# Kernel tuning notes

Measured on AMD Instinct MI355X. Metric: run time of the kernel, lower is better.

The kernel has to match this reference:

```python
import jax, jax.numpy as jnp
import numpy as np

BN_EPS = 1e-5


def _spe_forward(feature, neigh_idx, W, gamma, beta, running_mean, running_var):
    # feature: [B, C, N, 1]; neigh_idx: [B, N, K]
    B = feature.shape[0]
    pc = jnp.transpose(feature[..., 0], (0, 2, 1))            # [B, N, C]
    # gather neighbor features: [B, N, K, C]
    f_neigh = pc[jnp.arange(B)[:, None, None], neigh_idx]
    f_neigh = jnp.transpose(f_neigh, (0, 3, 1, 2))            # [B, C, N, K]
    f = jnp.concatenate((feature, f_neigh), axis=-1)          # [B, C, N, K+1]
    # 1x1 conv (no bias, followed by BN)
    h = jnp.einsum('oc,bcnk->bonk', W, f)                     # [B, O, N, K+1]
    # BatchNorm2d (eval mode with running stats) + ReLU
    inv = gamma / jnp.sqrt(running_var + BN_EPS)
    h = h * inv[None, :, None, None] + (beta - running_mean * inv)[None, :, None, None]
    h = jax.nn.relu(h)
    # sum over the neighbor axis, keepdim
    return jnp.sum(h, axis=-1, keepdims=True)                 # [B, O, N, 1]


def setup_inputs() -> dict:
    key = jax.random.key(0)
    k1, k2, k3 = jax.random.split(key, 3)
    B, C, N, K, O = 2, 64, 32768, 16, 64
    feature = jax.random.normal(k1, (B, C, N, 1), dtype=jnp.float32)
    neigh_idx = jax.random.randint(k2, (B, N, K), 0, N, dtype=jnp.int32)
    W = jax.random.normal(k3, (O, C), dtype=jnp.float32) * (1.0 / np.sqrt(C))
    gamma = jnp.ones((O,), dtype=jnp.float32)
    beta = jnp.zeros((O,), dtype=jnp.float32)
    running_mean = jnp.zeros((O,), dtype=jnp.float32)
    running_var = jnp.ones((O,), dtype=jnp.float32)
    return {"feature": feature, "neigh_idx": neigh_idx, "W": W,
            "gamma": gamma, "beta": beta,
            "running_mean": running_mean, "running_var": running_var}


def reference(feature, neigh_idx, W, gamma, beta, running_mean, running_var):
    return _spe_forward(feature, neigh_idx, W, gamma, beta, running_mean, running_var)
```

## Files before the change

kernel.cpp:

```cpp
#include <hip/hip_runtime.h>

#define BN_EPS 1e-5f

constexpr int Bb = 2;
constexpr int Cc = 64;
constexpr int Nn = 32768;
constexpr int Kk = 16;
constexpr int Oo = 64;

typedef __attribute__((ext_vector_type(8))) short v8s;
typedef __attribute__((ext_vector_type(4))) float v4f;

__device__ __forceinline__ unsigned short f2bf(float f) {
    unsigned u = __float_as_uint(f);
    return (unsigned short)((u + 0x7FFFu + ((u >> 16) & 1u)) >> 16);
}
__device__ __forceinline__ float bf2f(unsigned short h) {
    return __uint_as_float(((unsigned)h) << 16);
}

__global__ __launch_bounds__(256) void spe_gemm_mfma(
    const float* __restrict__ feature, const float* __restrict__ W,
    const float* __restrict__ gamma, const float* __restrict__ beta,
    const float* __restrict__ rmean, const float* __restrict__ rvar,
    unsigned short* __restrict__ t)
{
    __shared__ unsigned short fA[64][68];
    __shared__ unsigned short fB[64][68];
    const int tid = threadIdx.x;
    const int blk = blockIdx.x;
    const int b   = blk & 1;
    const int n0  = (blk >> 1) << 6;

    {
        const int nl = tid & 63;
        const int h  = tid >> 6;
        const float* fp = feature + (size_t)b * Cc * Nn + n0 + nl;
        #pragma unroll
        for (int i = 0; i < 16; ++i) {
            const int c = h * 16 + i;
            fA[nl][c] = f2bf(fp[(size_t)c * Nn]);
        }
        const int c2 = tid & 63;
        #pragma unroll
        for (int i = 0; i < 16; ++i) {
            const int o = h + i * 4;
            fB[o][c2] = f2bf(W[o * 64 + c2]);
        }
    }
    __syncthreads();

    const int wv   = tid >> 6;
    const int lane = tid & 63;
    const int q    = lane >> 4;
    const int r16  = lane & 15;

    union U8 { ushort4 u4[2]; v8s v; };
    const int am = wv * 16 + r16;
    U8 a0, a1;
    a0.u4[0] = *(const ushort4*)&fA[am][q * 8];
    a0.u4[1] = *(const ushort4*)&fA[am][q * 8 + 4];
    a1.u4[0] = *(const ushort4*)&fA[am][32 + q * 8];
    a1.u4[1] = *(const ushort4*)&fA[am][32 + q * 8 + 4];

    v4f acc[4];
    #pragma unroll
    for (int ot = 0; ot < 4; ++ot) {
        const int bo = ot * 16 + r16;
        U8 b0, b1;
        b0.u4[0] = *(const ushort4*)&fB[bo][q * 8];
        b0.u4[1] = *(const ushort4*)&fB[bo][q * 8 + 4];
        b1.u4[0] = *(const ushort4*)&fB[bo][32 + q * 8];
        b1.u4[1] = *(const ushort4*)&fB[bo][32 + q * 8 + 4];
        v4f c = {0.f, 0.f, 0.f, 0.f};
        c = __builtin_amdgcn_mfma_f32_16x16x32_bf16(a0.v, b0.v, c, 0, 0, 0);
        c = __builtin_amdgcn_mfma_f32_16x16x32_bf16(a1.v, b1.v, c, 0, 0, 0);
        acc[ot] = c;
    }

    #pragma unroll
    for (int ot = 0; ot < 4; ++ot) {
        const int o = ot * 16 + r16;
        const float inv  = gamma[o] / sqrtf(rvar[o] + BN_EPS);
        const float bias = beta[o] - rmean[o] * inv;
        unsigned short* tp = t + ((size_t)b * Nn + n0 + wv * 16 + q * 4) * 64 + o;
        #pragma unroll
        for (int r = 0; r < 4; ++r)
            tp[(size_t)r * 64] = f2bf(fmaxf(fmaf(inv, acc[ot][r], bias), 0.0f));
    }
}

__global__ __launch_bounds__(1024) void spe_gather_sum(
    const unsigned short* __restrict__ t, const int* __restrict__ idx,
    float* __restrict__ out)
{
    __shared__ float s[64 * 65];
    const int tid  = threadIdx.x;
    const int wv   = tid >> 6;
    const int lane = tid & 63;
    const int p    = lane >> 4;
    const int q    = lane & 15;
    const int blk  = blockIdx.x;
    const int b    = blk & 1;
    const int n0   = ((blk >> 1) & 511) << 6;
    const int ng   = n0 + wv * 4;

    const unsigned short* tb = t + (size_t)b * Nn * 64;

    const int myidx = idx[((size_t)b * Nn + ng) * Kk + lane];

    const int n = ng + p;
    const ushort4 c4 = *(const ushort4*)&tb[(size_t)n * 64 + q * 4];
    float ax = bf2f(c4.x), ay = bf2f(c4.y), az = bf2f(c4.z), aw = bf2f(c4.w);
    #pragma unroll
    for (int j = 0; j < 16; ++j) {
        const int nj = __shfl(myidx, p * 16 + j);
        const ushort4 v = *(const ushort4*)&tb[(size_t)nj * 64 + q * 4];
        ax += bf2f(v.x); ay += bf2f(v.y); az += bf2f(v.z); aw += bf2f(v.w);
    }

    const int nl = wv * 4 + p;
    float* sp = &s[nl * 65 + q * 4];
    sp[0] = ax; sp[1] = ay; sp[2] = az; sp[3] = aw;
    __syncthreads();

    const int nl2 = tid & 63;
    const int ob  = tid >> 6;
    float* op = out + (size_t)b * Oo * Nn + n0 + nl2;
    #pragma unroll
    for (int i = 0; i < 4; ++i) {
        const int o = ob * 4 + i;
        op[(size_t)o * Nn] = s[nl2 * 65 + o];
    }
}

extern "C" void kernel_launch(void* const* d_in, const int* in_sizes, int n_in,
                              void* d_out, int out_size, void* d_ws, size_t ws_size,
                              hipStream_t stream) {
    const float* feature = (const float*)d_in[0];
    const int*   nidx    = (const int*)d_in[1];
    const float* W       = (const float*)d_in[2];
    const float* gamma   = (const float*)d_in[3];
    const float* beta    = (const float*)d_in[4];
    const float* rmean   = (const float*)d_in[5];
    const float* rvar    = (const float*)d_in[6];
    float* out = (float*)d_out;
    unsigned short* t = (unsigned short*)d_ws;

    const int nblocks = Bb * (Nn / 64);
    spe_gemm_mfma<<<nblocks, 256, 0, stream>>>(feature, W, gamma, beta, rmean, rvar, t);
    spe_gather_sum<<<nblocks, 1024, 0, stream>>>(t, nidx, out);
}
```

Baseline: 95.53 us.

## Load GEMM operands directly to registers and widen gather rows to 16 bytes

The GEMM kernel no longer stages feature and W through shared memory. Each lane loads its MFMA fragments straight from global memory, with swapped operand roles so that output rows are written as packed ushort4 stores, and the BN parameters are read as float4. The gather kernel now uses 512 threads with 8 lanes per point, each lane loading 16-byte rows, and issues all 17 loads before accumulating to raise memory-level parallelism. This trades shared-memory staging and a barrier for more redundant global reads of W and higher register pressure from holding 17 uint4 values per lane.

```diff
diff --git a/kernel.cpp b/kernel.cpp
--- a/kernel.cpp
+++ b/kernel.cpp
@@ -15,9 +15,6 @@
     unsigned u = __float_as_uint(f);
     return (unsigned short)((u + 0x7FFFu + ((u >> 16) & 1u)) >> 16);
 }
-__device__ __forceinline__ float bf2f(unsigned short h) {
-    return __uint_as_float(((unsigned)h) << 16);
-}
 
 __global__ __launch_bounds__(256) void spe_gemm_mfma(
     const float* __restrict__ feature, const float* __restrict__ W,
@@ -25,72 +22,62 @@
     const float* __restrict__ rmean, const float* __restrict__ rvar,
     unsigned short* __restrict__ t)
 {
-    __shared__ unsigned short fA[64][68];
-    __shared__ unsigned short fB[64][68];
     const int tid = threadIdx.x;
     const int blk = blockIdx.x;
     const int b   = blk & 1;
     const int n0  = (blk >> 1) << 6;
-
-    {
-        const int nl = tid & 63;
-        const int h  = tid >> 6;
-        const float* fp = feature + (size_t)b * Cc * Nn + n0 + nl;
-        #pragma unroll
-        for (int i = 0; i < 16; ++i) {
-            const int c = h * 16 + i;
-            fA[nl][c] = f2bf(fp[(size_t)c * Nn]);
-        }
-        const int c2 = tid & 63;
-        #pragma unroll
-        for (int i = 0; i < 16; ++i) {
-            const int o = h + i * 4;
-            fB[o][c2] = f2bf(W[o * 64 + c2]);
-        }
-    }
-    __syncthreads();
 
     const int wv   = tid >> 6;
     const int lane = tid & 63;
     const int q    = lane >> 4;
     const int r16  = lane & 15;
 
-    union U8 { ushort4 u4[2]; v8s v; };
-    const int am = wv * 16 + r16;
-    U8 a0, a1;
-    a0.u4[0] = *(const ushort4*)&fA[am][q * 8];
-    a0.u4[1] = *(const ushort4*)&fA[am][q * 8 + 4];
-    a1.u4[0] = *(const ushort4*)&fA[am][32 + q * 8];
-    a1.u4[1] = *(const ushort4*)&fA[am][32 + q * 8 + 4];
+    union U { ushort4 u4[2]; unsigned short us[8]; v8s v; };
 
-    v4f acc[4];
+    const int nb = n0 + wv * 16 + r16;
+    const float* fp = feature + (size_t)b * Cc * Nn + nb;
+    U bf0, bf1;
     #pragma unroll
-    for (int ot = 0; ot < 4; ++ot) {
-        const int bo = ot * 16 + r16;
-        U8 b0, b1;
-        b0.u4[0] = *(const ushort4*)&fB[bo][q * 8];
-        b0.u4[1] = *(const ushort4*)&fB[bo][q * 8 + 4];
-        b1.u4[0] = *(const ushort4*)&fB[bo][32 + q * 8];
-        b1.u4[1] = *(const ushort4*)&fB[bo][32 + q * 8 + 4];
-        v4f c = {0.f, 0.f, 0.f, 0.f};
-        c = __builtin_amdgcn_mfma_f32_16x16x32_bf16(a0.v, b0.v, c, 0, 0, 0);
-        c = __builtin_amdgcn_mfma_f32_16x16x32_bf16(a1.v, b1.v, c, 0, 0, 0);
-        acc[ot] = c;
+    for (int jj = 0; jj < 8; ++jj) {
+        bf0.us[jj] = f2bf(fp[(size_t)(q * 8 + jj) * Nn]);
+        bf1.us[jj] = f2bf(fp[(size_t)(q * 8 + jj + 32) * Nn]);
     }
 
     #pragma unroll
     for (int ot = 0; ot < 4; ++ot) {
-        const int o = ot * 16 + r16;
-        const float inv  = gamma[o] / sqrtf(rvar[o] + BN_EPS);
-        const float bias = beta[o] - rmean[o] * inv;
-        unsigned short* tp = t + ((size_t)b * Nn + n0 + wv * 16 + q * 4) * 64 + o;
+        const int oa = ot * 16 + r16;
+        const float* wp = W + oa * 64 + q * 8;
+        U af0, af1;
         #pragma unroll
-        for (int r = 0; r < 4; ++r)
-            tp[(size_t)r * 64] = f2bf(fmaxf(fmaf(inv, acc[ot][r], bias), 0.0f));
+        for (int jj = 0; jj < 8; ++jj) {
+            af0.us[jj] = f2bf(wp[jj]);
+            af1.us[jj] = f2bf(wp[jj + 32]);
+        }
+        v4f c = {0.f, 0.f, 0.f, 0.f};
+        c = __builtin_amdgcn_mfma_f32_16x16x32_bf16(af0.v, bf0.v, c, 0, 0, 0);
+        c = __builtin_amdgcn_mfma_f32_16x16x32_bf16(af1.v, bf1.v, c, 0, 0, 0);
+
+        const int ob4 = ot * 16 + q * 4;
+        const float4 g4  = *(const float4*)&gamma[ob4];
+        const float4 be4 = *(const float4*)&beta[ob4];
+        const float4 m4  = *(const float4*)&rmean[ob4];
+        const float4 v4  = *(const float4*)&rvar[ob4];
+        float inv[4], bias[4];
+        inv[0] = g4.x / sqrtf(v4.x + BN_EPS);  bias[0] = be4.x - m4.x * inv[0];
+        inv[1] = g4.y / sqrtf(v4.y + BN_EPS);  bias[1] = be4.y - m4.y * inv[1];
+        inv[2] = g4.z / sqrtf(v4.z + BN_EPS);  bias[2] = be4.z - m4.z * inv[2];
+        inv[3] = g4.w / sqrtf(v4.w + BN_EPS);  bias[3] = be4.w - m4.w * inv[3];
+
+        ushort4 ov;
+        ov.x = f2bf(fmaxf(fmaf(inv[0], c[0], bias[0]), 0.0f));
+        ov.y = f2bf(fmaxf(fmaf(inv[1], c[1], bias[1]), 0.0f));
+        ov.z = f2bf(fmaxf(fmaf(inv[2], c[2], bias[2]), 0.0f));
+        ov.w = f2bf(fmaxf(fmaf(inv[3], c[3], bias[3]), 0.0f));
+        *(ushort4*)&t[((size_t)b * Nn + nb) * 64 + ob4] = ov;
     }
 }
 
-__global__ __launch_bounds__(1024) void spe_gather_sum(
+__global__ __launch_bounds__(512, 4) void spe_gather_sum(
     const unsigned short* __restrict__ t, const int* __restrict__ idx,
     float* __restrict__ out)
 {
@@ -98,38 +85,51 @@
     const int tid  = threadIdx.x;
     const int wv   = tid >> 6;
     const int lane = tid & 63;
-    const int p    = lane >> 4;
-    const int q    = lane & 15;
+    const int p    = lane >> 3;
+    const int e    = lane & 7;
     const int blk  = blockIdx.x;
     const int b    = blk & 1;
-    const int n0   = ((blk >> 1) & 511) << 6;
-    const int ng   = n0 + wv * 4;
+    const int n0   = (blk >> 1) << 6;
+    const int ng   = n0 + wv * 8;
 
     const unsigned short* tb = t + (size_t)b * Nn * 64;
 
-    const int myidx = idx[((size_t)b * Nn + ng) * Kk + lane];
+    const int2 mi = ((const int2*)(idx + ((size_t)b * Nn + ng) * Kk))[lane];
 
     const int n = ng + p;
-    const ushort4 c4 = *(const ushort4*)&tb[(size_t)n * 64 + q * 4];
-    float ax = bf2f(c4.x), ay = bf2f(c4.y), az = bf2f(c4.z), aw = bf2f(c4.w);
+    uint4 v[17];
+    v[0] = *(const uint4*)&tb[(size_t)n * 64 + e * 8];
     #pragma unroll
     for (int j = 0; j < 16; ++j) {
-        const int nj = __shfl(myidx, p * 16 + j);
-        const ushort4 v = *(const ushort4*)&tb[(size_t)nj * 64 + q * 4];
-        ax += bf2f(v.x); ay += bf2f(v.y); az += bf2f(v.z); aw += bf2f(v.w);
+        const int src = p * 8 + (j >> 1);
+        const int nj  = __shfl((j & 1) ? mi.y : mi.x, src);
+        v[j + 1] = *(const uint4*)&tb[(size_t)nj * 64 + e * 8];
     }
 
-    const int nl = wv * 4 + p;
-    float* sp = &s[nl * 65 + q * 4];
-    sp[0] = ax; sp[1] = ay; sp[2] = az; sp[3] = aw;
+    float acc[8] = {0.f, 0.f, 0.f, 0.f, 0.f, 0.f, 0.f, 0.f};
+    #pragma unroll
+    for (int j = 0; j < 17; ++j) {
+        acc[0] += __uint_as_float(v[j].x << 16);
+        acc[1] += __uint_as_float(v[j].x & 0xFFFF0000u);
+        acc[2] += __uint_as_float(v[j].y << 16);
+        acc[3] += __uint_as_float(v[j].y & 0xFFFF0000u);
+        acc[4] += __uint_as_float(v[j].z << 16);
+        acc[5] += __uint_as_float(v[j].z & 0xFFFF0000u);
+        acc[6] += __uint_as_float(v[j].w << 16);
+        acc[7] += __uint_as_float(v[j].w & 0xFFFF0000u);
+    }
+
+    float* sp = &s[(wv * 8 + p) * 65 + e * 8];
+    #pragma unroll
+    for (int i = 0; i < 8; ++i) sp[i] = acc[i];
     __syncthreads();
 
     const int nl2 = tid & 63;
     const int ob  = tid >> 6;
     float* op = out + (size_t)b * Oo * Nn + n0 + nl2;
     #pragma unroll
-    for (int i = 0; i < 4; ++i) {
-        const int o = ob * 4 + i;
+    for (int i = 0; i < 8; ++i) {
+        const int o = ob * 8 + i;
         op[(size_t)o * Nn] = s[nl2 * 65 + o];
     }
 }
@@ -149,5 +149,5 @@
 
     const int nblocks = Bb * (Nn / 64);
     spe_gemm_mfma<<<nblocks, 256, 0, stream>>>(feature, W, gamma, beta, rmean, rvar, t);
-    spe_gather_sum<<<nblocks, 1024, 0, stream>>>(t, nidx, out);
+    spe_gather_sum<<<nblocks, 512, 0, stream>>>(t, nidx, out);
 }
```

Result: slower. 100.5 us (+5.2%).
